# Optimization experiments

Hardware: AMD Instinct MI355X
Metric: run time of the kernel (lower is better)

The kernel has to match this reference:

```python
import jax, jax.numpy as jnp
import numpy as np

EMB = 64
D = 2 * EMB          # 128, feature dim of R / hidden of attention MLP
B, L = 128, 4096     # batch, sequence length
N_ITER = 50          # bisection iterations (entmax_bisect default)


def entmax_bisect(X, alpha, n_iter=N_ITER):
    """alpha-entmax via bisection over the last axis. X: [B, L], alpha: [B, 1] (>1)."""
    am1 = alpha - 1.0
    Xs = X * am1
    d = X.shape[-1]
    inv = 1.0 / am1
    max_val = jnp.max(Xs, axis=-1, keepdims=True)
    tau_lo0 = max_val - 1.0                       # gp(1, alpha) = 1
    tau_hi = max_val - (1.0 / d) ** am1           # gp(1/d, alpha)

    def p(tau):
        return jnp.clip(Xs - tau, 0.0, None) ** inv

    f_lo = jnp.sum(p(tau_lo0), axis=-1, keepdims=True) - 1.0

    def body(i, carry):
        tau_lo, dm, _ = carry
        dm = dm * 0.5
        tau_m = tau_lo + dm
        f_m = jnp.sum(p(tau_m), axis=-1, keepdims=True) - 1.0
        tau_lo = jnp.where(f_m * f_lo >= 0, tau_m, tau_lo)
        return (tau_lo, dm, tau_m)

    _, _, tau_m = jax.lax.fori_loop(0, n_iter, body, (tau_lo0, tau_hi - tau_lo0, tau_lo0))
    p_m = p(tau_m)
    return p_m / jnp.sum(p_m, axis=-1, keepdims=True)  # ensure_sum_one


def setup_inputs() -> dict:
    key = jax.random.key(0)
    ks = jax.random.split(key, 9)
    s = 1.0 / np.sqrt(D)
    R = jax.random.normal(ks[0], (B, L, D), dtype=jnp.float32)
    alpha = 1.25 + 0.5 * jax.random.uniform(ks[1], (B, 1), dtype=jnp.float32)  # in (1.25, 1.75)
    target = jax.random.normal(ks[2], (B, 1, D), dtype=jnp.float32)
    Wr1 = s * jax.random.normal(ks[3], (D, D), dtype=jnp.float32)      # Linear(2E, 2E), no bias
    Wr2 = s * jax.random.normal(ks[4], (D, EMB), dtype=jnp.float32)    # Linear(E, 2E) (shape-fixed), no bias
    Wr3 = s * jax.random.normal(ks[5], (1, D), dtype=jnp.float32)      # Linear(2E, 1), no bias
    bias_r = s * jax.random.normal(ks[6], (D,), dtype=jnp.float32)
    Wf_w = s * jax.random.normal(ks[7], (EMB, D), dtype=jnp.float32)   # Linear(2E, E)
    Wf_b = s * jax.random.normal(ks[8], (EMB,), dtype=jnp.float32)
    return {"R": R, "alpha": alpha, "target": target, "Wr1": Wr1, "Wr2": Wr2,
            "Wr3": Wr3, "bias_r": bias_r, "Wf_w": Wf_w, "Wf_b": Wf_b}


def reference(R, alpha, target, Wr1, Wr2, Wr3, bias_r, Wf_w, Wf_b):
    # q = Wf(target): [B, 1, E]
    q = jnp.einsum('btd,ed->bte', target, Wf_w) + Wf_b
    # additive attention score: Wr3 @ relu(Wr1 k + Wr2 q + b): [B, L]
    h = jax.nn.relu(jnp.einsum('bld,ed->ble', R, Wr1)
                    + jnp.einsum('bte,de->btd', q, Wr2)
                    + bias_r)
    scores = jnp.einsum('bld,d->bl', h, Wr3[0])
    # entmax sparsification over the sequence axis
    a = entmax_bisect(scores, alpha)
    # weighted sum of v = R: [B, D]
    res = jnp.einsum('bl,bld->bd', a, R)
    res = jax.nn.selu(res)
    res = res / jnp.linalg.norm(res, axis=-1, keepdims=True)
    return res
```

## Files before the change

kernel.cpp:

```cpp
#include <hip/hip_runtime.h>
#include <hip/hip_bf16.h>

#define B_ 128
#define L_ 4096
#define D_ 128
#define E_ 64

typedef __attribute__((ext_vector_type(8))) short short8;
typedef __attribute__((ext_vector_type(4))) float floatx4;

static __device__ __forceinline__ unsigned short f2bf(float x) {
  __hip_bfloat16 h = __float2bfloat16(x);
  union { __hip_bfloat16 h; unsigned short u; } c; c.h = h; return c.u;
}
static __device__ __forceinline__ float bf2f(unsigned short u) {
  union { unsigned short u; __hip_bfloat16 h; } c; c.u = u; return __bfloat162float(c.h);
}

__global__ __launch_bounds__(128) void pass_a(
    const float* __restrict__ target, const float* __restrict__ Wr2,
    const float* __restrict__ bias_r, const float* __restrict__ Wf_w,
    const float* __restrict__ Wf_b, float* __restrict__ cvec) {
  const int b = blockIdx.x, t = threadIdx.x;
  __shared__ float tg[D_];
  __shared__ float q[E_];
  tg[t] = target[b * D_ + t];
  __syncthreads();
  if (t < E_) {
    float s = Wf_b[t];
    #pragma unroll 8
    for (int d = 0; d < D_; ++d) s += tg[d] * Wf_w[t * D_ + d];
    q[t] = s;
  }
  __syncthreads();
  float s = bias_r[t];
  #pragma unroll 8
  for (int e = 0; e < E_; ++e) s += q[e] * Wr2[t * E_ + e];
  cvec[b * D_ + t] = s;
}

__global__ __launch_bounds__(256) void wr1_split(const float* __restrict__ Wr1,
    unsigned short* __restrict__ hi, unsigned short* __restrict__ lo) {
  int t = blockIdx.x * 256 + threadIdx.x;
  int j = t & 7, lane = (t >> 3) & 63, ks = (t >> 9) & 3, nt = t >> 11;
  int e = nt * 16 + (lane & 15);
  int d = ks * 32 + (lane >> 4) * 8 + j;
  float x = Wr1[e * D_ + d];
  unsigned short h = f2bf(x);
  hi[t] = h;
  lo[t] = f2bf(x - bf2f(h));
}

__global__ __launch_bounds__(256, 2) void pass_b(
    const float* __restrict__ R, const unsigned short* __restrict__ Whi,
    const unsigned short* __restrict__ Wlo, const float* __restrict__ cvec,
    const float* __restrict__ Wr3, float* __restrict__ scores) {
  __shared__ __align__(16) unsigned short sAhi[16384];
  __shared__ __align__(16) unsigned short sAlo[16384];
  const int b = blockIdx.x >> 5;
  const int lt = blockIdx.x & 31;
  const int t = threadIdx.x;
  const int wave = t >> 6, lane = t & 63;
  const int col = lane & 15, quad = lane >> 4;

  const float* Rbase = R + ((size_t)b * L_ + (size_t)lt * 128) * D_;
  #pragma unroll
  for (int i = 0; i < 8; ++i) {
    const int mt = wave * 2 + (i >> 2);
    const int ks = i & 3;
    const int row = mt * 16 + (lane & 15);
    const int c0 = ks * 32 + (lane >> 4) * 8;
    const float4* p = (const float4*)(Rbase + (size_t)row * D_ + c0);
    float4 v0 = p[0], v1 = p[1];
    float vv[8] = {v0.x, v0.y, v0.z, v0.w, v1.x, v1.y, v1.z, v1.w};
    union { unsigned short u[8]; short8 v; } H, Lo;
    #pragma unroll
    for (int j = 0; j < 8; ++j) {
      unsigned short h = f2bf(vv[j]);
      H.u[j] = h;
      Lo.u[j] = f2bf(vv[j] - bf2f(h));
    }
    const int base = ((mt * 4 + ks) * 64 + lane) * 8;
    *(short8*)(sAhi + base) = H.v;
    *(short8*)(sAlo + base) = Lo.v;
  }

  short8 bh[2][4], bl[2][4];
  #pragma unroll
  for (int n = 0; n < 2; ++n)
    #pragma unroll
    for (int ks = 0; ks < 4; ++ks) {
      int off = (((wave * 2 + n) * 4 + ks) * 64 + lane) * 8;
      bh[n][ks] = *(const short8*)(Whi + off);
      bl[n][ks] = *(const short8*)(Wlo + off);
    }

  floatx4 acc[8][2];
  #pragma unroll
  for (int mt = 0; mt < 8; ++mt)
    #pragma unroll
    for (int n = 0; n < 2; ++n) acc[mt][n] = (floatx4){0.f, 0.f, 0.f, 0.f};

  __syncthreads();

  #pragma unroll
  for (int mt = 0; mt < 8; ++mt) {
    #pragma unroll
    for (int ks = 0; ks < 4; ++ks) {
      int ai = ((mt * 4 + ks) * 64 + lane) * 8;
      short8 ah = *(const short8*)(sAhi + ai);
      short8 al = *(const short8*)(sAlo + ai);
      #pragma unroll
      for (int n = 0; n < 2; ++n) {
        acc[mt][n] = __builtin_amdgcn_mfma_f32_16x16x32_bf16(ah, bh[n][ks], acc[mt][n], 0, 0, 0);
        acc[mt][n] = __builtin_amdgcn_mfma_f32_16x16x32_bf16(al, bh[n][ks], acc[mt][n], 0, 0, 0);
        acc[mt][n] = __builtin_amdgcn_mfma_f32_16x16x32_bf16(ah, bl[n][ks], acc[mt][n], 0, 0, 0);
      }
    }
  }

  float w3[2], cb[2];
  #pragma unroll
  for (int n = 0; n < 2; ++n) {
    int e = (wave * 2 + n) * 16 + col;
    w3[n] = Wr3[e];
    cb[n] = cvec[b * D_ + e];
  }
  float part[8][4];
  #pragma unroll
  for (int mt = 0; mt < 8; ++mt)
    #pragma unroll
    for (int r = 0; r < 4; ++r) {
      float s = 0.f;
      #pragma unroll
      for (int n = 0; n < 2; ++n)
        s += w3[n] * fmaxf(acc[mt][n][r] + cb[n], 0.f);
      s += __shfl_xor(s, 1, 64);
      s += __shfl_xor(s, 2, 64);
      s += __shfl_xor(s, 4, 64);
      s += __shfl_xor(s, 8, 64);
      part[mt][r] = s;
    }
  __syncthreads();
  float* red = (float*)sAhi;
  if (col == 0) {
    #pragma unroll
    for (int mt = 0; mt < 8; ++mt)
      #pragma unroll
      for (int r = 0; r < 4; ++r)
        red[wave * 128 + mt * 16 + quad * 4 + r] = part[mt][r];
  }
  __syncthreads();
  if (t < 128) {
    float s = (red[t] + red[128 + t]) + (red[256 + t] + red[384 + t]);
    scores[(size_t)b * L_ + lt * 128 + t] = s;
  }
}

__global__ __launch_bounds__(512) void pass_cd(
    const float* __restrict__ scores, const float* __restrict__ alpha,
    const float* __restrict__ R, float* __restrict__ out) {
  const int b = blockIdx.x, t = threadIdx.x;
  const int wave = t >> 6, lane = t & 63;
  __shared__ float sred[2][8];
  __shared__ unsigned short sidx[L_];
  __shared__ float sw[L_];
  __shared__ float ppart[512];
  __shared__ int scnt;
  const float am1 = alpha[b] - 1.0f;
  const float inv = 1.0f / am1;
  const float* S = scores + (size_t)b * L_;
  float Xs[8];
  #pragma unroll
  for (int i = 0; i < 8; ++i) Xs[i] = S[i * 512 + t] * am1;
  if (t == 0) scnt = 0;

  float mx = Xs[0];
  #pragma unroll
  for (int i = 1; i < 8; ++i) mx = fmaxf(mx, Xs[i]);
  #pragma unroll
  for (int m = 32; m >= 1; m >>= 1) mx = fmaxf(mx, __shfl_xor(mx, m, 64));
  if (lane == 0) sred[0][wave] = mx;
  __syncthreads();
  mx = sred[0][0];
  #pragma unroll
  for (int w = 1; w < 8; ++w) mx = fmaxf(mx, sred[0][w]);

  float tau_lo = mx - 1.0f;
  float tau_hi = mx - exp2f(-12.0f * am1);
  float dm = tau_hi - tau_lo;

  int pc = 1;
  auto sumP = [&](float tau) -> float {
    const int par = pc & 1;
    ++pc;
    float s = 0.f;
    #pragma unroll
    for (int i = 0; i < 8; ++i) {
      float u = Xs[i] - tau;
      if (u > 0.f) s += exp2f(inv * __log2f(u));
    }
    #pragma unroll
    for (int m = 32; m >= 1; m >>= 1) s += __shfl_xor(s, m, 64);
    if (lane == 0) sred[par][wave] = s;
    __syncthreads();
    float r = sred[par][0];
    #pragma unroll
    for (int w = 1; w < 8; ++w) r += sred[par][w];
    return r;
  };

  const float f_lo = sumP(tau_lo) - 1.0f;
  float tau_m = tau_lo;
  for (int it = 0; it < 40; ++it) {
    dm *= 0.5f;
    tau_m = tau_lo + dm;
    float f_m = sumP(tau_m) - 1.0f;
    if (f_m * f_lo >= 0.f) tau_lo = tau_m;
  }

  float p[8];
  float s = 0.f;
  #pragma unroll
  for (int i = 0; i < 8; ++i) {
    float u = Xs[i] - tau_m;
    p[i] = (u > 0.f) ? exp2f(inv * __log2f(u)) : 0.f;
    s += p[i];
  }
  {
    const int par = pc & 1;
    ++pc;
    float ss = s;
    #pragma unroll
    for (int m = 32; m >= 1; m >>= 1) ss += __shfl_xor(ss, m, 64);
    if (lane == 0) sred[par][wave] = ss;
    __syncthreads();
    s = sred[par][0];
    #pragma unroll
    for (int w = 1; w < 8; ++w) s += sred[par][w];
  }
  const float rs = 1.0f / s;
  #pragma unroll
  for (int i = 0; i < 8; ++i) {
    if (p[i] > 0.f) {
      int pos = atomicAdd(&scnt, 1);
      sidx[pos] = (unsigned short)(i * 512 + t);
      sw[pos] = p[i] * rs;
    }
  }
  __syncthreads();
  const int n = scnt;

  const float* Rb = R + (size_t)b * L_ * D_;
  const int g = t >> 7, c = t & 127;
  float acc = 0.f;
  int k = g;
  for (; k + 4 < n; k += 8) {
    int i0 = sidx[k], i1 = sidx[k + 4];
    float w0 = sw[k], w1 = sw[k + 4];
    acc += w0 * Rb[(size_t)i0 * D_ + c] + w1 * Rb[(size_t)i1 * D_ + c];
  }
  for (; k < n; k += 4) acc += sw[k] * Rb[(size_t)sidx[k] * D_ + c];
  __syncthreads();
  ppart[t] = acc;
  __syncthreads();
  float r = 0.f;
  if (t < 128) {
    float a2 = (ppart[t] + ppart[t + 128]) + (ppart[t + 256] + ppart[t + 384]);
    const float sc = 1.0507009873554805f, al = 1.6732632423543772f;
    r = a2 > 0.f ? sc * a2 : sc * al * (expf(a2) - 1.0f);
  }
  float q = r * r;
  #pragma unroll
  for (int m = 32; m >= 1; m >>= 1) q += __shfl_xor(q, m, 64);
  if (lane == 0) sred[0][wave] = q;
  __syncthreads();
  if (t < 128) {
    float nrm = sqrtf(sred[0][0] + sred[0][1]);
    out[b * D_ + t] = r / nrm;
  }
}

extern "C" void kernel_launch(void* const* d_in, const int* in_sizes, int n_in,
                              void* d_out, int out_size, void* d_ws, size_t ws_size,
                              hipStream_t stream) {
  const float* R      = (const float*)d_in[0];
  const float* alpha  = (const float*)d_in[1];
  const float* target = (const float*)d_in[2];
  const float* Wr1    = (const float*)d_in[3];
  const float* Wr2    = (const float*)d_in[4];
  const float* Wr3    = (const float*)d_in[5];
  const float* bias_r = (const float*)d_in[6];
  const float* Wf_w   = (const float*)d_in[7];
  const float* Wf_b   = (const float*)d_in[8];
  float* out = (float*)d_out;

  char* ws = (char*)d_ws;
  float* cvec          = (float*)ws;
  unsigned short* whi  = (unsigned short*)(ws + 65536);
  unsigned short* wlo  = (unsigned short*)(ws + 98304);
  float* scores        = (float*)(ws + 131072);

  hipLaunchKernelGGL(pass_a, dim3(B_), dim3(128), 0, stream,
                     target, Wr2, bias_r, Wf_w, Wf_b, cvec);
  hipLaunchKernelGGL(wr1_split, dim3(64), dim3(256), 0, stream, Wr1, whi, wlo);
  hipLaunchKernelGGL(pass_b, dim3(B_ * 32), dim3(256), 0, stream,
                     R, whi, wlo, cvec, Wr3, scores);
  hipLaunchKernelGGL(pass_cd, dim3(B_), dim3(512), 0, stream,
                     scores, alpha, R, out);
}
```

Baseline: 458.1 us.

## Compact entmax candidates before bisection and merge prep kernels

Before bisection, the entmax kernel gathers only the elements above the initial lower threshold (max-1) into shared memory. Each of the 40 bisection iterations then evaluates the power function over that shorter candidate list instead of all 4096 elements. The final normalization is applied after the weighted sum, and the sparse index list is built in the final pass. Separately, the query projection and the Wr1 bf16 split are fused into one launch to save a kernel launch. The cost is extra shared memory and a strided loop over a variable-length list, and the atomic compaction makes the summation order nondeterministic.

```diff
diff --git a/kernel.cpp b/kernel.cpp
--- a/kernel.cpp
+++ b/kernel.cpp
@@ -17,38 +17,41 @@
   union { unsigned short u; __hip_bfloat16 h; } c; c.u = u; return __bfloat162float(c.h);
 }
 
-__global__ __launch_bounds__(128) void pass_a(
-    const float* __restrict__ target, const float* __restrict__ Wr2,
-    const float* __restrict__ bias_r, const float* __restrict__ Wf_w,
-    const float* __restrict__ Wf_b, float* __restrict__ cvec) {
-  const int b = blockIdx.x, t = threadIdx.x;
-  __shared__ float tg[D_];
-  __shared__ float q[E_];
-  tg[t] = target[b * D_ + t];
-  __syncthreads();
-  if (t < E_) {
-    float s = Wf_b[t];
+__global__ __launch_bounds__(256) void prep(
+    const float* __restrict__ Wr1, unsigned short* __restrict__ hi,
+    unsigned short* __restrict__ lo, const float* __restrict__ target,
+    const float* __restrict__ Wr2, const float* __restrict__ bias_r,
+    const float* __restrict__ Wf_w, const float* __restrict__ Wf_b,
+    float* __restrict__ cvec) {
+  if (blockIdx.x < 64) {
+    int t = blockIdx.x * 256 + threadIdx.x;
+    int j = t & 7, lane = (t >> 3) & 63, ks = (t >> 9) & 3, nt = t >> 11;
+    int e = nt * 16 + (lane & 15);
+    int d = ks * 32 + (lane >> 4) * 8 + j;
+    float x = Wr1[e * D_ + d];
+    unsigned short h = f2bf(x);
+    hi[t] = h;
+    lo[t] = f2bf(x - bf2f(h));
+  } else {
+    const int sub = threadIdx.x >> 7;
+    const int t = threadIdx.x & 127;
+    const int b = (blockIdx.x - 64) * 2 + sub;
+    __shared__ float tg[2][D_];
+    __shared__ float q[2][E_];
+    tg[sub][t] = target[b * D_ + t];
+    __syncthreads();
+    if (t < E_) {
+      float s = Wf_b[t];
+      #pragma unroll 8
+      for (int d = 0; d < D_; ++d) s += tg[sub][d] * Wf_w[t * D_ + d];
+      q[sub][t] = s;
+    }
+    __syncthreads();
+    float s = bias_r[t];
     #pragma unroll 8
-    for (int d = 0; d < D_; ++d) s += tg[d] * Wf_w[t * D_ + d];
-    q[t] = s;
-  }
-  __syncthreads();
-  float s = bias_r[t];
-  #pragma unroll 8
-  for (int e = 0; e < E_; ++e) s += q[e] * Wr2[t * E_ + e];
-  cvec[b * D_ + t] = s;
-}
-
-__global__ __launch_bounds__(256) void wr1_split(const float* __restrict__ Wr1,
-    unsigned short* __restrict__ hi, unsigned short* __restrict__ lo) {
-  int t = blockIdx.x * 256 + threadIdx.x;
-  int j = t & 7, lane = (t >> 3) & 63, ks = (t >> 9) & 3, nt = t >> 11;
-  int e = nt * 16 + (lane & 15);
-  int d = ks * 32 + (lane >> 4) * 8 + j;
-  float x = Wr1[e * D_ + d];
-  unsigned short h = f2bf(x);
-  hi[t] = h;
-  lo[t] = f2bf(x - bf2f(h));
+    for (int e = 0; e < E_; ++e) s += q[sub][e] * Wr2[t * E_ + e];
+    cvec[b * D_ + t] = s;
+  }
 }
 
 __global__ __launch_bounds__(256, 2) void pass_b(
@@ -162,18 +165,20 @@
     const float* __restrict__ R, float* __restrict__ out) {
   const int b = blockIdx.x, t = threadIdx.x;
   const int wave = t >> 6, lane = t & 63;
+  __shared__ float sX[L_];
+  __shared__ unsigned short sI[L_];
+  __shared__ float sW[L_];
+  __shared__ unsigned short sJ[L_];
+  __shared__ float ppart[512];
   __shared__ float sred[2][8];
-  __shared__ unsigned short sidx[L_];
-  __shared__ float sw[L_];
-  __shared__ float ppart[512];
-  __shared__ int scnt;
+  __shared__ int scnt, smcnt;
   const float am1 = alpha[b] - 1.0f;
   const float inv = 1.0f / am1;
   const float* S = scores + (size_t)b * L_;
   float Xs[8];
   #pragma unroll
   for (int i = 0; i < 8; ++i) Xs[i] = S[i * 512 + t] * am1;
-  if (t == 0) scnt = 0;
+  if (t == 0) { scnt = 0; smcnt = 0; }
 
   float mx = Xs[0];
   #pragma unroll
@@ -186,18 +191,28 @@
   #pragma unroll
   for (int w = 1; w < 8; ++w) mx = fmaxf(mx, sred[0][w]);
 
-  float tau_lo = mx - 1.0f;
-  float tau_hi = mx - exp2f(-12.0f * am1);
-  float dm = tau_hi - tau_lo;
+  const float tau_lo0 = mx - 1.0f;
+  #pragma unroll
+  for (int i = 0; i < 8; ++i) {
+    if (Xs[i] > tau_lo0) {
+      int pos = atomicAdd(&scnt, 1);
+      sX[pos] = Xs[i];
+      sI[pos] = (unsigned short)(i * 512 + t);
+    }
+  }
+  __syncthreads();
+  const int n = scnt;
+
+  float tau_lo = tau_lo0;
+  float dm = (mx - exp2f(-12.0f * am1)) - tau_lo;
 
   int pc = 1;
   auto sumP = [&](float tau) -> float {
     const int par = pc & 1;
     ++pc;
     float s = 0.f;
-    #pragma unroll
-    for (int i = 0; i < 8; ++i) {
-      float u = Xs[i] - tau;
+    for (int k = t; k < n; k += 512) {
+      float u = sX[k] - tau;
       if (u > 0.f) s += exp2f(inv * __log2f(u));
     }
     #pragma unroll
@@ -219,54 +234,47 @@
     if (f_m * f_lo >= 0.f) tau_lo = tau_m;
   }
 
-  float p[8];
   float s = 0.f;
-  #pragma unroll
-  for (int i = 0; i < 8; ++i) {
-    float u = Xs[i] - tau_m;
-    p[i] = (u > 0.f) ? exp2f(inv * __log2f(u)) : 0.f;
-    s += p[i];
+  for (int k = t; k < n; k += 512) {
+    float u = sX[k] - tau_m;
+    if (u > 0.f) {
+      float p = exp2f(inv * __log2f(u));
+      s += p;
+      int pos = atomicAdd(&smcnt, 1);
+      sJ[pos] = sI[k];
+      sW[pos] = p;
+    }
   }
   {
     const int par = pc & 1;
     ++pc;
-    float ss = s;
-    #pragma unroll
-    for (int m = 32; m >= 1; m >>= 1) ss += __shfl_xor(ss, m, 64);
-    if (lane == 0) sred[par][wave] = ss;
+    #pragma unroll
+    for (int m = 32; m >= 1; m >>= 1) s += __shfl_xor(s, m, 64);
+    if (lane == 0) sred[par][wave] = s;
     __syncthreads();
     s = sred[par][0];
     #pragma unroll
     for (int w = 1; w < 8; ++w) s += sred[par][w];
   }
+  const int ns = smcnt;
   const float rs = 1.0f / s;
-  #pragma unroll
-  for (int i = 0; i < 8; ++i) {
-    if (p[i] > 0.f) {
-      int pos = atomicAdd(&scnt, 1);
-      sidx[pos] = (unsigned short)(i * 512 + t);
-      sw[pos] = p[i] * rs;
-    }
-  }
-  __syncthreads();
-  const int n = scnt;
 
   const float* Rb = R + (size_t)b * L_ * D_;
   const int g = t >> 7, c = t & 127;
   float acc = 0.f;
   int k = g;
-  for (; k + 4 < n; k += 8) {
-    int i0 = sidx[k], i1 = sidx[k + 4];
-    float w0 = sw[k], w1 = sw[k + 4];
+  for (; k + 4 < ns; k += 8) {
+    int i0 = sJ[k], i1 = sJ[k + 4];
+    float w0 = sW[k], w1 = sW[k + 4];
     acc += w0 * Rb[(size_t)i0 * D_ + c] + w1 * Rb[(size_t)i1 * D_ + c];
   }
-  for (; k < n; k += 4) acc += sw[k] * Rb[(size_t)sidx[k] * D_ + c];
+  for (; k < ns; k += 4) acc += sW[k] * Rb[(size_t)sJ[k] * D_ + c];
   __syncthreads();
   ppart[t] = acc;
   __syncthreads();
   float r = 0.f;
   if (t < 128) {
-    float a2 = (ppart[t] + ppart[t + 128]) + (ppart[t + 256] + ppart[t + 384]);
+    float a2 = ((ppart[t] + ppart[t + 128]) + (ppart[t + 256] + ppart[t + 384])) * rs;
     const float sc = 1.0507009873554805f, al = 1.6732632423543772f;
     r = a2 > 0.f ? sc * a2 : sc * al * (expf(a2) - 1.0f);
   }
@@ -301,9 +309,8 @@
   unsigned short* wlo  = (unsigned short*)(ws + 98304);
   float* scores        = (float*)(ws + 131072);
 
-  hipLaunchKernelGGL(pass_a, dim3(B_), dim3(128), 0, stream,
-                     target, Wr2, bias_r, Wf_w, Wf_b, cvec);
-  hipLaunchKernelGGL(wr1_split, dim3(64), dim3(256), 0, stream, Wr1, whi, wlo);
+  hipLaunchKernelGGL(prep, dim3(128), dim3(256), 0, stream,
+                     Wr1, whi, wlo, target, Wr2, bias_r, Wf_w, Wf_b, cvec);
   hipLaunchKernelGGL(pass_b, dim3(B_ * 32), dim3(256), 0, stream,
                      R, whi, wlo, cvec, Wr3, scores);
   hipLaunchKernelGGL(pass_cd, dim3(B_), dim3(512), 0, stream,
```

Result: slower. 468.3 us (+2.2%).
